# Kernel optimization log

Measured on AMD Instinct MI355X. Metric: run time of the kernel, lower is better.

Reference implementation:

```python
import jax, jax.numpy as jnp
import numpy as np

B, N, D = 2, 2048, 2048
H, I, K, V = 16, 1, 128, 128
EPS = 1e-6


def setup_inputs() -> dict:
    key = jax.random.key(0)
    ks = jax.random.split(key, 6)
    x_q = jax.random.normal(ks[0], (B, N, D), dtype=jnp.float32)
    # norm_mask: lower-triangular causal mask (the 'nm' operand); values in [0,1]
    norm_mask = jnp.tril(jax.random.uniform(ks[1], (N, N), dtype=jnp.float32))
    scale = 1.0 / np.sqrt(D)
    w_q = jax.random.normal(ks[2], (D, H, I, K), dtype=jnp.float32) * scale
    w_k = jax.random.normal(ks[3], (D, H, K), dtype=jnp.float32) * scale
    w_v = jax.random.normal(ks[4], (D, H, V), dtype=jnp.float32) * scale
    w_o = jax.random.normal(ks[5], (H, I, V, D), dtype=jnp.float32) * (1.0 / np.sqrt(H * I * V))
    rms_scale = jnp.ones((V,), dtype=jnp.float32)
    return {"x_q": x_q, "norm_mask": norm_mask, "w_q": w_q, "w_k": w_k,
            "w_v": w_v, "rms_scale": rms_scale, "w_o": w_o}


def reference(x_q, norm_mask, w_q, w_k, w_v, rms_scale, w_o):
    # self-attention: x_k = x_v = x_q
    q = jnp.einsum('bnd,dhik->bnhik', x_q, w_q)   # (B,N,H,I,K)
    k = jnp.einsum('bnd,dhk->bnhk', x_q, w_k)     # (B,N,H,K)
    v = jnp.einsum('bnd,dhv->bnhv', x_q, w_v)     # (B,N,H,V)
    # linear (no-softmax) attention with decay/normalization mask 'nm'
    s = jnp.einsum('bnhik,bmhk->bnhim', q, k)     # (B,N,H,I,N)
    s = s * norm_mask[None, :, None, None, :]
    y = jnp.einsum('bnhim,bmhv->bnhiv', s, v)     # (B,N,H,I,V)
    # RMSNorm over v_head_d
    ms = jnp.mean(jnp.square(y), axis=-1, keepdims=True)
    y = y * jax.lax.rsqrt(ms + EPS) * rms_scale
    # output projection
    return jnp.einsum('bnhiv,hivd->bnd', y, w_o)
```

## Files before the change

kernel.cpp:

```cpp
#include <hip/hip_runtime.h>
#include <hip/hip_bf16.h>


typedef _Float16 f16x8 __attribute__((ext_vector_type(8)));
typedef _Float16 f16x4 __attribute__((ext_vector_type(4)));
typedef float    f32x4 __attribute__((ext_vector_type(4)));

#define DEV static __device__ __forceinline__

DEV int swzx(int row) { return (((row & 7) ^ ((row >> 3) & 7)) << 4); }

typedef const unsigned int __attribute__((address_space(1)))* gas_t;
typedef unsigned int __attribute__((address_space(3)))* las_t;
DEV void gld16(const void* g, void* l) {
  __builtin_amdgcn_global_load_lds((gas_t)g, (las_t)l, 16, 0, 0);
}

__global__ void k_cast_h(const float* __restrict__ in, _Float16* __restrict__ out, int n) {
  int i = (blockIdx.x * blockDim.x + threadIdx.x) * 4;
  int stride = gridDim.x * blockDim.x * 4;
  for (; i < n; i += stride) {
    float4 v = *reinterpret_cast<const float4*>(in + i);
    f16x4 o;
    o[0] = (_Float16)v.x; o[1] = (_Float16)v.y;
    o[2] = (_Float16)v.z; o[3] = (_Float16)v.w;
    *reinterpret_cast<f16x4*>(out + i) = o;
  }
}

__global__ void k_transpose_h(const float* __restrict__ in, _Float16* __restrict__ out) {
  __shared__ float tile[32][33];
  int tx = threadIdx.x, ty = threadIdx.y;
  int c0 = blockIdx.x * 32, r0 = blockIdx.y * 32;
  #pragma unroll
  for (int j = 0; j < 4; ++j)
    tile[ty + j * 8][tx] = in[(size_t)(r0 + ty + j * 8) * 2048 + c0 + tx];
  __syncthreads();
  #pragma unroll
  for (int j = 0; j < 4; ++j)
    out[(size_t)(c0 + ty + j * 8) * 2048 + r0 + tx] = (_Float16)tile[tx][ty + j * 8];
}

__global__ void k_transpose_v(const _Float16* __restrict__ in, _Float16* __restrict__ out) {
  __shared__ _Float16 tile[32][33];
  int tx = threadIdx.x, ty = threadIdx.y;
  int v0 = blockIdx.x * 32, n0 = blockIdx.y * 32, bh = blockIdx.z;
  int b = bh >> 4, h = bh & 15;
  #pragma unroll
  for (int j = 0; j < 4; ++j)
    tile[ty + j * 8][tx] =
        in[(size_t)(b * 2048 + n0 + ty + j * 8) * 6144 + 4096 + h * 128 + v0 + tx];
  __syncthreads();
  #pragma unroll
  for (int j = 0; j < 4; ++j)
    out[((size_t)bh * 128 + v0 + ty + j * 8) * 2048 + n0 + tx] = tile[tx][ty + j * 8];
}

template <int OUTF32>
__global__ __launch_bounds__(256) void k_gemm1(const _Float16* __restrict__ A,
                                               const _Float16* __restrict__ B,
                                               void* __restrict__ C, int ldc) {
  __shared__ __align__(16) _Float16 As[128 * 64];
  __shared__ __align__(16) _Float16 Bs[128 * 64];
  const int tid = threadIdx.x;
  const int lane = tid & 63, w = tid >> 6;
  const int lr = lane & 15, lg = lane >> 4;
  const int bm = blockIdx.y, bn = blockIdx.x;
  const int wr = (w >> 1) * 64, wc = (w & 1) * 64;

  f32x4 acc[4][4];
  #pragma unroll
  for (int i = 0; i < 4; ++i)
    #pragma unroll
    for (int j = 0; j < 4; ++j) { f32x4 z = {0.f, 0.f, 0.f, 0.f}; acc[i][j] = z; }

  const size_t aOff = (size_t)(bm * 128) * 2048;
  const size_t bOff = (size_t)(bn * 128) * 2048;

  for (int kt = 0; kt < 32; ++kt) {
    __syncthreads();
    #pragma unroll
    for (int it = 0; it < 4; ++it) {
      int row = it * 32 + (tid >> 3);
      int cb  = ((tid & 7) * 16) ^ swzx(row);
      size_t g = (size_t)row * 2048 + kt * 64 + (cb >> 1);
      int ld = it * 4096 + tid * 16;
      gld16(A + aOff + g, (char*)As + ld);
      gld16(B + bOff + g, (char*)Bs + ld);
    }
    __syncthreads();
    #pragma unroll
    for (int ks = 0; ks < 2; ++ks) {
      f16x8 af[4], bf[4];
      #pragma unroll
      for (int f = 0; f < 4; ++f) {
        int ar = wr + f * 16 + lr;
        af[f] = *reinterpret_cast<const f16x8*>((const char*)As + ar * 128 +
                                                ((ks * 64 + lg * 16) ^ swzx(ar)));
        int br = wc + f * 16 + lr;
        bf[f] = *reinterpret_cast<const f16x8*>((const char*)Bs + br * 128 +
                                                ((ks * 64 + lg * 16) ^ swzx(br)));
      }
      __builtin_amdgcn_s_setprio(1);
      #pragma unroll
      for (int i = 0; i < 4; ++i)
        #pragma unroll
        for (int j = 0; j < 4; ++j)
          acc[i][j] = __builtin_amdgcn_mfma_f32_16x16x32_f16(af[i], bf[j], acc[i][j], 0, 0, 0);
      __builtin_amdgcn_s_setprio(0);
    }
  }

  #pragma unroll
  for (int fm = 0; fm < 4; ++fm)
    #pragma unroll
    for (int fn = 0; fn < 4; ++fn)
      #pragma unroll
      for (int r = 0; r < 4; ++r) {
        int grow = bm * 128 + wr + fm * 16 + lg * 4 + r;
        int gcol = bn * 128 + wc + fn * 16 + lr;
        float v = acc[fm][fn][r];
        size_t o = (size_t)grow * ldc + gcol;
        if (OUTF32) ((float*)C)[o] = v;
        else        ((_Float16*)C)[o] = (_Float16)v;
      }
}

__global__ __launch_bounds__(256) void k_attn1(const _Float16* __restrict__ qkv,
                                               const _Float16* __restrict__ vt,
                                               const float* __restrict__ nm,
                                               const float* __restrict__ rms_scale,
                                               _Float16* __restrict__ y) {
  __shared__ __align__(16) _Float16 Ks[2][64 * 128];
  __shared__ __align__(16) _Float16 Vs[2][128 * 64];
  __shared__ __align__(16) _Float16 Ps[64 * 64];
  const int tid = threadIdx.x;
  const int lane = tid & 63, w = tid >> 6;
  const int lr = lane & 15, lg = lane >> 4;
  const int bh = blockIdx.x, b = bh >> 4, h = bh & 15;
  const _Float16* qb = qkv + (size_t)b * 2048 * 6144 + h * 128;
  const _Float16* kb = qkv + (size_t)b * 2048 * 6144 + 2048 + h * 128;
  const size_t vbase = (size_t)bh * 128 * 2048;

  const int krow = tid >> 4, kc = tid & 15;
  const int vrow = tid >> 3, vc = tid & 7;

  auto STAGE = [&](int t, int bufi) {
    #pragma unroll
    for (int it = 0; it < 4; ++it) {
      int kr = it * 16 + krow;
      int gk = ((kc * 16) ^ swzx(kr)) >> 1;
      gld16(kb + (size_t)(t * 64 + kr) * 6144 + gk,
            (char*)Ks[bufi] + it * 4096 + tid * 16);
      int vr = it * 32 + vrow;
      int gv = ((vc * 16) ^ swzx(vr)) >> 1;
      gld16(vt + vbase + (size_t)vr * 2048 + t * 64 + gv,
            (char*)Vs[bufi] + it * 4096 + tid * 16);
    }
  };

  #pragma unroll
  for (int pi = 0; pi < 2; ++pi) {
    const int qt = pi ? (31 - (int)blockIdx.y) : (int)blockIdx.y;
    const int nT = qt + 1;

    f16x8 aq[4];
    {
      const _Float16* qrow = qb + (size_t)(qt * 64 + w * 16 + lr) * 6144;
      #pragma unroll
      for (int ks = 0; ks < 4; ++ks)
        aq[ks] = *reinterpret_cast<const f16x8*>(qrow + ks * 32 + lg * 8);
    }

    f32x4 accY[8];
    #pragma unroll
    for (int i = 0; i < 8; ++i) { f32x4 z = {0.f, 0.f, 0.f, 0.f}; accY[i] = z; }

    STAGE(0, 0);
    asm volatile("s_waitcnt vmcnt(0)" ::: "memory");
    __builtin_amdgcn_s_barrier();
    __builtin_amdgcn_sched_barrier(0);

    for (int t = 0; t < nT; ++t) {
      const int cur = t & 1;

      float nmv[4][4];
      #pragma unroll
      for (int fm = 0; fm < 4; ++fm)
        #pragma unroll
        for (int r = 0; r < 4; ++r)
          nmv[fm][r] = nm[(size_t)(qt * 64 + w * 16 + lg * 4 + r) * 2048 +
                          t * 64 + fm * 16 + lr];
      __builtin_amdgcn_sched_barrier(0);

      if (t + 1 < nT) STAGE(t + 1, cur ^ 1);

      f32x4 accS[4];
      #pragma unroll
      for (int i = 0; i < 4; ++i) { f32x4 z = {0.f, 0.f, 0.f, 0.f}; accS[i] = z; }
      __builtin_amdgcn_s_setprio(1);
      #pragma unroll
      for (int ks = 0; ks < 4; ++ks) {
        #pragma unroll
        for (int fm = 0; fm < 4; ++fm) {
          int br = fm * 16 + lr;
          f16x8 bk = *reinterpret_cast<const f16x8*>(
              (const char*)Ks[cur] + br * 256 + ((ks * 64 + lg * 16) ^ swzx(br)));
          accS[fm] = __builtin_amdgcn_mfma_f32_16x16x32_f16(aq[ks], bk, accS[fm], 0, 0, 0);
        }
      }
      __builtin_amdgcn_s_setprio(0);

      #pragma unroll
      for (int fm = 0; fm < 4; ++fm)
        #pragma unroll
        for (int r = 0; r < 4; ++r) {
          float pv = accS[fm][r] * nmv[fm][r];
          int pr = w * 16 + lg * 4 + r, pc = fm * 16 + lr;
          *reinterpret_cast<_Float16*>((char*)Ps + pr * 128 + ((pc * 2) ^ swzx(pr))) =
              (_Float16)pv;
        }

      __builtin_amdgcn_s_setprio(1);
      #pragma unroll
      for (int ks = 0; ks < 2; ++ks) {
        int ar = w * 16 + lr;
        f16x8 ap = *reinterpret_cast<const f16x8*>(
            (const char*)Ps + ar * 128 + ((ks * 64 + lg * 16) ^ swzx(ar)));
        #pragma unroll
        for (int fv = 0; fv < 8; ++fv) {
          int br = fv * 16 + lr;
          f16x8 bv = *reinterpret_cast<const f16x8*>(
              (const char*)Vs[cur] + br * 128 + ((ks * 64 + lg * 16) ^ swzx(br)));
          accY[fv] = __builtin_amdgcn_mfma_f32_16x16x32_f16(ap, bv, accY[fv], 0, 0, 0);
        }
      }
      __builtin_amdgcn_s_setprio(0);

      asm volatile("s_waitcnt vmcnt(0)" ::: "memory");
      __builtin_amdgcn_s_barrier();
      __builtin_amdgcn_sched_barrier(0);
    }

    #pragma unroll
    for (int r = 0; r < 4; ++r) {
      float sq = 0.f;
      #pragma unroll
      for (int fv = 0; fv < 8; ++fv) { float yy = accY[fv][r]; sq += yy * yy; }
      sq += __shfl_xor(sq, 1); sq += __shfl_xor(sq, 2);
      sq += __shfl_xor(sq, 4); sq += __shfl_xor(sq, 8);
      float scale = rsqrtf(sq * (1.0f / 128.0f) + 1e-6f);
      int nrow = qt * 64 + w * 16 + lg * 4 + r;
      size_t orow = ((size_t)b * 2048 + nrow) * 2048 + (size_t)h * 128;
      #pragma unroll
      for (int fv = 0; fv < 8; ++fv) {
        int col = fv * 16 + lr;
        y[orow + col] = (_Float16)(accY[fv][r] * scale * rms_scale[col]);
      }
    }
  }
}

extern "C" void kernel_launch(void* const* d_in, const int* in_sizes, int n_in,
                              void* d_out, int out_size, void* d_ws, size_t ws_size,
                              hipStream_t stream) {
  (void)in_sizes; (void)n_in; (void)out_size; (void)ws_size;
  const float* x  = (const float*)d_in[0];
  const float* nm = (const float*)d_in[1];
  const float* wq = (const float*)d_in[2];
  const float* wk = (const float*)d_in[3];
  const float* wv = (const float*)d_in[4];
  const float* rs = (const float*)d_in[5];
  const float* wo = (const float*)d_in[6];

  _Float16* p = (_Float16*)d_ws;
  _Float16* xf  = p; p += 8388608;
  _Float16* wt3 = p; p += 12582912;
  _Float16* wto = p; p += 4194304;
  _Float16* qkv = p; p += 25165824;
  _Float16* vtf = p; p += 8388608;

  k_cast_h<<<dim3(2048), dim3(256), 0, stream>>>(x, xf, 8388608);

  k_transpose_h<<<dim3(64, 64), dim3(32, 8), 0, stream>>>(wq, wt3);
  k_transpose_h<<<dim3(64, 64), dim3(32, 8), 0, stream>>>(wk, wt3 + 4194304);
  k_transpose_h<<<dim3(64, 64), dim3(32, 8), 0, stream>>>(wv, wt3 + 8388608);
  k_transpose_h<<<dim3(64, 64), dim3(32, 8), 0, stream>>>(wo, wto);

  k_gemm1<0><<<dim3(48, 32), dim3(256), 0, stream>>>(xf, wt3, qkv, 6144);
  k_transpose_v<<<dim3(4, 64, 32), dim3(32, 8), 0, stream>>>(qkv, vtf);

  k_attn1<<<dim3(32, 16), dim3(256), 0, stream>>>(qkv, vtf, nm, rs, xf);

  k_gemm1<1><<<dim3(16, 32), dim3(256), 0, stream>>>(xf, wto, d_out, 2048);
}
```

Baseline: 283.9 us.

## Use 256x256 double-buffered QKV GEMM and merge weight transposes into one launch

Adds a new QKV projection GEMM with 256x256 tiles, 512 threads, double-buffered LDS staging through global_load_lds, and a swizzled layout. Larger tiles give more operand reuse per LDS load and overlap the next k-tile's loads with the MFMAs. The four weight transpose launches are merged into a single launch that picks its input by blockIdx.z, which removes launch overhead. Only 384 blocks run for the QKV GEMM, which may underfill the 256 CUs, and the large LDS footprint allows just one block per CU.

```diff
diff --git a/kernel.cpp b/kernel.cpp
--- a/kernel.cpp
+++ b/kernel.cpp
@@ -28,8 +28,18 @@
   }
 }
 
-__global__ void k_transpose_h(const float* __restrict__ in, _Float16* __restrict__ out) {
+__global__ void k_transpose_h4(const float* __restrict__ w0, const float* __restrict__ w1,
+                               const float* __restrict__ w2, const float* __restrict__ w3,
+                               _Float16* __restrict__ o0, _Float16* __restrict__ o1,
+                               _Float16* __restrict__ o2, _Float16* __restrict__ o3) {
   __shared__ float tile[32][33];
+  const float* in; _Float16* out;
+  switch (blockIdx.z) {
+    case 0: in = w0; out = o0; break;
+    case 1: in = w1; out = o1; break;
+    case 2: in = w2; out = o2; break;
+    default: in = w3; out = o3; break;
+  }
   int tx = threadIdx.x, ty = threadIdx.y;
   int c0 = blockIdx.x * 32, r0 = blockIdx.y * 32;
   #pragma unroll
@@ -56,10 +66,100 @@
     out[((size_t)bh * 128 + v0 + ty + j * 8) * 2048 + n0 + tx] = tile[tx][ty + j * 8];
 }
 
-template <int OUTF32>
+__global__ __launch_bounds__(512) void k_gemm256(const _Float16* __restrict__ A,
+                                                 const _Float16* __restrict__ B,
+                                                 _Float16* __restrict__ C, int ldc) {
+  __shared__ __align__(16) _Float16 Ab[2][256 * 64];
+  __shared__ __align__(16) _Float16 Bb[2][256 * 64];
+  const int tid = threadIdx.x;
+  const int lane = tid & 63, w = tid >> 6;
+  const int lr = lane & 15, lg = lane >> 4;
+  const int bm = blockIdx.y, bn = blockIdx.x;
+  const int wr = (w >> 2) * 128, wc = (w & 3) * 64;
+
+  f32x4 acc[8][4];
+  #pragma unroll
+  for (int i = 0; i < 8; ++i)
+    #pragma unroll
+    for (int j = 0; j < 4; ++j) { f32x4 z = {0.f, 0.f, 0.f, 0.f}; acc[i][j] = z; }
+
+  const _Float16* aBase = A + (size_t)(bm * 256) * 2048;
+  const _Float16* bBase = B + (size_t)(bn * 256) * 2048;
+
+  const int srow = tid >> 3, sc8 = tid & 7;
+
+  auto STAGE = [&](int kt, int bufi) {
+    #pragma unroll
+    for (int it = 0; it < 4; ++it) {
+      int row = it * 64 + srow;
+      int cb  = (sc8 * 16) ^ swzx(row);
+      size_t g = (size_t)row * 2048 + kt * 64 + (cb >> 1);
+      int ld = it * 8192 + tid * 16;
+      gld16(aBase + g, (char*)Ab[bufi] + ld);
+      gld16(bBase + g, (char*)Bb[bufi] + ld);
+    }
+  };
+
+  STAGE(0, 0);
+  asm volatile("s_waitcnt vmcnt(0)" ::: "memory");
+  __builtin_amdgcn_s_barrier();
+  __builtin_amdgcn_sched_barrier(0);
+
+  for (int kt = 0; kt < 32; ++kt) {
+    const int cur = kt & 1;
+    if (kt + 1 < 32) STAGE(kt + 1, cur ^ 1);
+    __builtin_amdgcn_sched_barrier(0);
+
+    f16x8 bf[4];
+    #pragma unroll
+    for (int p = 0; p < 4; ++p) {
+      const int ks = p >> 1, mh = p & 1;
+      if (mh == 0) {
+        #pragma unroll
+        for (int nj = 0; nj < 4; ++nj) {
+          int br = wc + nj * 16 + lr;
+          bf[nj] = *reinterpret_cast<const f16x8*>(
+              (const char*)Bb[cur] + br * 128 + ((ks * 64 + lg * 16) ^ swzx(br)));
+        }
+      }
+      f16x8 af[4];
+      #pragma unroll
+      for (int m4 = 0; m4 < 4; ++m4) {
+        int ar = wr + mh * 64 + m4 * 16 + lr;
+        af[m4] = *reinterpret_cast<const f16x8*>(
+            (const char*)Ab[cur] + ar * 128 + ((ks * 64 + lg * 16) ^ swzx(ar)));
+      }
+      __builtin_amdgcn_s_setprio(1);
+      #pragma unroll
+      for (int m4 = 0; m4 < 4; ++m4)
+        #pragma unroll
+        for (int nj = 0; nj < 4; ++nj)
+          acc[mh * 4 + m4][nj] =
+              __builtin_amdgcn_mfma_f32_16x16x32_f16(af[m4], bf[nj], acc[mh * 4 + m4][nj], 0, 0, 0);
+      __builtin_amdgcn_s_setprio(0);
+      __builtin_amdgcn_sched_barrier(0);
+    }
+
+    asm volatile("s_waitcnt vmcnt(0)" ::: "memory");
+    __builtin_amdgcn_s_barrier();
+    __builtin_amdgcn_sched_barrier(0);
+  }
+
+  #pragma unroll
+  for (int mi = 0; mi < 8; ++mi)
+    #pragma unroll
+    for (int nj = 0; nj < 4; ++nj)
+      #pragma unroll
+      for (int r = 0; r < 4; ++r) {
+        int grow = bm * 256 + wr + mi * 16 + lg * 4 + r;
+        int gcol = bn * 256 + wc + nj * 16 + lr;
+        C[(size_t)grow * ldc + gcol] = (_Float16)acc[mi][nj][r];
+      }
+}
+
 __global__ __launch_bounds__(256) void k_gemm1(const _Float16* __restrict__ A,
                                                const _Float16* __restrict__ B,
-                                               void* __restrict__ C, int ldc) {
+                                               float* __restrict__ C, int ldc) {
   __shared__ __align__(16) _Float16 As[128 * 64];
   __shared__ __align__(16) _Float16 Bs[128 * 64];
   const int tid = threadIdx.x;
@@ -119,10 +219,7 @@
       for (int r = 0; r < 4; ++r) {
         int grow = bm * 128 + wr + fm * 16 + lg * 4 + r;
         int gcol = bn * 128 + wc + fn * 16 + lr;
-        float v = acc[fm][fn][r];
-        size_t o = (size_t)grow * ldc + gcol;
-        if (OUTF32) ((float*)C)[o] = v;
-        else        ((_Float16*)C)[o] = (_Float16)v;
+        C[(size_t)grow * ldc + gcol] = acc[fm][fn][r];
       }
 }
 
@@ -282,15 +379,13 @@
 
   k_cast_h<<<dim3(2048), dim3(256), 0, stream>>>(x, xf, 8388608);
 
-  k_transpose_h<<<dim3(64, 64), dim3(32, 8), 0, stream>>>(wq, wt3);
-  k_transpose_h<<<dim3(64, 64), dim3(32, 8), 0, stream>>>(wk, wt3 + 4194304);
-  k_transpose_h<<<dim3(64, 64), dim3(32, 8), 0, stream>>>(wv, wt3 + 8388608);
-  k_transpose_h<<<dim3(64, 64), dim3(32, 8), 0, stream>>>(wo, wto);
-
-  k_gemm1<0><<<dim3(48, 32), dim3(256), 0, stream>>>(xf, wt3, qkv, 6144);
+  k_transpose_h4<<<dim3(64, 64, 4), dim3(32, 8), 0, stream>>>(
+      wq, wk, wv, wo, wt3, wt3 + 4194304, wt3 + 8388608, wto);
+
+  k_gemm256<<<dim3(24, 16), dim3(512), 0, stream>>>(xf, wt3, qkv, 6144);
   k_transpose_v<<<dim3(4, 64, 32), dim3(32, 8), 0, stream>>>(qkv, vtf);
 
   k_attn1<<<dim3(32, 16), dim3(256), 0, stream>>>(qkv, vtf, nm, rs, xf);
 
-  k_gemm1<1><<<dim3(16, 32), dim3(256), 0, stream>>>(xf, wto, d_out, 2048);
-}
+  k_gemm1<<<dim3(16, 32), dim3(256), 0, stream>>>(xf, wto, (float*)d_out, 2048);
+}
```

Result: no change. 288.6 us (+1.7%).

## Double-buffer GEMM LDS tiles and merge four weight transposes into one launch

Applied to the files above, without the earlier changes.

The GEMM kernel now uses two LDS buffers: it issues the global-to-LDS loads for the next k-tile before running MFMAs on the current one, with a single waitcnt and barrier per iteration instead of two syncthreads. This is meant to hide global load latency behind compute. It doubles LDS use to 64KB per block, which may lower occupancy. The four weight transpose launches are folded into one kernel indexed by blockIdx.z to cut launch overhead.

```diff
diff --git a/kernel.cpp b/kernel.cpp
--- a/kernel.cpp
+++ b/kernel.cpp
@@ -28,8 +28,18 @@
   }
 }
 
-__global__ void k_transpose_h(const float* __restrict__ in, _Float16* __restrict__ out) {
+__global__ void k_transpose_h4(const float* __restrict__ w0, const float* __restrict__ w1,
+                               const float* __restrict__ w2, const float* __restrict__ w3,
+                               _Float16* __restrict__ o0, _Float16* __restrict__ o1,
+                               _Float16* __restrict__ o2, _Float16* __restrict__ o3) {
   __shared__ float tile[32][33];
+  const float* in; _Float16* out;
+  switch (blockIdx.z) {
+    case 0: in = w0; out = o0; break;
+    case 1: in = w1; out = o1; break;
+    case 2: in = w2; out = o2; break;
+    default: in = w3; out = o3; break;
+  }
   int tx = threadIdx.x, ty = threadIdx.y;
   int c0 = blockIdx.x * 32, r0 = blockIdx.y * 32;
   #pragma unroll
@@ -57,11 +67,11 @@
 }
 
 template <int OUTF32>
-__global__ __launch_bounds__(256) void k_gemm1(const _Float16* __restrict__ A,
-                                               const _Float16* __restrict__ B,
-                                               void* __restrict__ C, int ldc) {
-  __shared__ __align__(16) _Float16 As[128 * 64];
-  __shared__ __align__(16) _Float16 Bs[128 * 64];
+__global__ __launch_bounds__(256) void k_gemm_db(const _Float16* __restrict__ A,
+                                                 const _Float16* __restrict__ B,
+                                                 void* __restrict__ C, int ldc) {
+  __shared__ __align__(16) _Float16 As[2][128 * 64];
+  __shared__ __align__(16) _Float16 Bs[2][128 * 64];
   const int tid = threadIdx.x;
   const int lane = tid & 63, w = tid >> 6;
   const int lr = lane & 15, lg = lane >> 4;
@@ -77,28 +87,38 @@
   const size_t aOff = (size_t)(bm * 128) * 2048;
   const size_t bOff = (size_t)(bn * 128) * 2048;
 
-  for (int kt = 0; kt < 32; ++kt) {
-    __syncthreads();
+  auto STAGE = [&](int kt, int bufi) {
     #pragma unroll
     for (int it = 0; it < 4; ++it) {
       int row = it * 32 + (tid >> 3);
       int cb  = ((tid & 7) * 16) ^ swzx(row);
       size_t g = (size_t)row * 2048 + kt * 64 + (cb >> 1);
       int ld = it * 4096 + tid * 16;
-      gld16(A + aOff + g, (char*)As + ld);
-      gld16(B + bOff + g, (char*)Bs + ld);
-    }
-    __syncthreads();
+      gld16(A + aOff + g, (char*)As[bufi] + ld);
+      gld16(B + bOff + g, (char*)Bs[bufi] + ld);
+    }
+  };
+
+  STAGE(0, 0);
+  asm volatile("s_waitcnt vmcnt(0)" ::: "memory");
+  __builtin_amdgcn_s_barrier();
+  __builtin_amdgcn_sched_barrier(0);
+
+  for (int kt = 0; kt < 32; ++kt) {
+    const int cur = kt & 1;
+    if (kt + 1 < 32) STAGE(kt + 1, cur ^ 1);
+    __builtin_amdgcn_sched_barrier(0);
+
     #pragma unroll
     for (int ks = 0; ks < 2; ++ks) {
       f16x8 af[4], bf[4];
       #pragma unroll
       for (int f = 0; f < 4; ++f) {
         int ar = wr + f * 16 + lr;
-        af[f] = *reinterpret_cast<const f16x8*>((const char*)As + ar * 128 +
+        af[f] = *reinterpret_cast<const f16x8*>((const char*)As[cur] + ar * 128 +
                                                 ((ks * 64 + lg * 16) ^ swzx(ar)));
         int br = wc + f * 16 + lr;
-        bf[f] = *reinterpret_cast<const f16x8*>((const char*)Bs + br * 128 +
+        bf[f] = *reinterpret_cast<const f16x8*>((const char*)Bs[cur] + br * 128 +
                                                 ((ks * 64 + lg * 16) ^ swzx(br)));
       }
       __builtin_amdgcn_s_setprio(1);
@@ -109,6 +129,10 @@
           acc[i][j] = __builtin_amdgcn_mfma_f32_16x16x32_f16(af[i], bf[j], acc[i][j], 0, 0, 0);
       __builtin_amdgcn_s_setprio(0);
     }
+
+    asm volatile("s_waitcnt vmcnt(0)" ::: "memory");
+    __builtin_amdgcn_s_barrier();
+    __builtin_amdgcn_sched_barrier(0);
   }
 
   #pragma unroll
@@ -282,15 +306,13 @@
 
   k_cast_h<<<dim3(2048), dim3(256), 0, stream>>>(x, xf, 8388608);
 
-  k_transpose_h<<<dim3(64, 64), dim3(32, 8), 0, stream>>>(wq, wt3);
-  k_transpose_h<<<dim3(64, 64), dim3(32, 8), 0, stream>>>(wk, wt3 + 4194304);
-  k_transpose_h<<<dim3(64, 64), dim3(32, 8), 0, stream>>>(wv, wt3 + 8388608);
-  k_transpose_h<<<dim3(64, 64), dim3(32, 8), 0, stream>>>(wo, wto);
-
-  k_gemm1<0><<<dim3(48, 32), dim3(256), 0, stream>>>(xf, wt3, qkv, 6144);
+  k_transpose_h4<<<dim3(64, 64, 4), dim3(32, 8), 0, stream>>>(
+      wq, wk, wv, wo, wt3, wt3 + 4194304, wt3 + 8388608, wto);
+
+  k_gemm_db<0><<<dim3(48, 32), dim3(256), 0, stream>>>(xf, wt3, qkv, 6144);
   k_transpose_v<<<dim3(4, 64, 32), dim3(32, 8), 0, stream>>>(qkv, vtf);
 
   k_attn1<<<dim3(32, 16), dim3(256), 0, stream>>>(qkv, vtf, nm, rs, xf);
 
-  k_gemm1<1><<<dim3(16, 32), dim3(256), 0, stream>>>(xf, wto, d_out, 2048);
-}
+  k_gemm_db<1><<<dim3(16, 32), dim3(256), 0, stream>>>(xf, wto, d_out, 2048);
+}
```

Result: faster. 271.2 us, median of 2 (-4.4%).
